# Kernel tuning notes

Measured on AMD Instinct MI355X. Metric: run time of the kernel, lower is better.

## Reference

```python
import jax, jax.numpy as jnp
import numpy as np

PENETRATION_W = 10.0
STABILITY_W = 1.0
ENERGY_W = 0.1
MIN_DIST = 0.05

B, T, N, D = 16, 100, 128, 3

def setup_inputs() -> dict:
    key = jax.random.key(0)
    k1, k2, k3 = jax.random.split(key, 3)
    trajectories = jax.random.normal(k1, (B, T, N, D), dtype=jnp.float32)
    velocities = jax.random.normal(k2, (B, T, N, D), dtype=jnp.float32)
    forces = jax.random.normal(k3, (B, T, N, D), dtype=jnp.float32)
    return {"trajectories": trajectories, "velocities": velocities, "forces": forces}

def _penetration_loss(trajectories):
    b, t, n, _ = trajectories.shape
    pos = trajectories[..., :3]                                   # [B,T,N,3]
    diff = pos[:, :, :, None, :] - pos[:, :, None, :, :]          # [B,T,N,N,3]
    d2 = jnp.sum(diff * diff, axis=-1)                            # [B,T,N,N]
    mask = jnp.triu(jnp.ones((n, n), dtype=bool), k=1)            # strictly i<j
    # avoid sqrt(0) on diagonal for safe gradients; masked out below
    dist = jnp.sqrt(jnp.where(mask, d2, 1.0))
    pen = jax.nn.relu(MIN_DIST - dist) * mask                     # [B,T,N,N]
    # original: sum over (t, i<j) of mean over batch
    total = jnp.mean(jnp.sum(pen, axis=(1, 2, 3)))
    return total / (t * n * (n - 1) / 2)

def _stability_loss(velocities):
    return jnp.mean(jnp.linalg.norm(velocities[:, -5:], axis=-1))

def _energy_loss(positions, velocities, forces):
    kinetic_start = 0.5 * jnp.mean(jnp.sum(velocities[:, 0] ** 2, axis=-1))
    kinetic_end = 0.5 * jnp.mean(jnp.sum(velocities[:, -1] ** 2, axis=-1))
    displacements = positions[:, 1:] - positions[:, :-1]
    work = jnp.mean(jnp.sum(forces[:, :-1] * displacements, axis=-1))
    return jnp.abs(kinetic_end - kinetic_start - work)

def reference(trajectories, velocities, forces):
    loss = PENETRATION_W * _penetration_loss(trajectories)
    loss = loss + STABILITY_W * _stability_loss(velocities)
    loss = loss + ENERGY_W * _energy_loss(trajectories, velocities, forces)
    return loss
```

## Files before the change

### kernel.cpp

```cpp
#include <hip/hip_runtime.h>
#include <math.h>

constexpr int B = 16, T = 100, N = 128;
constexpr float MIN_DIST  = 0.05f;
constexpr float MIN_DIST2 = MIN_DIST * MIN_DIST;

constexpr int THREADS     = 256;
constexpr int MISC_BLOCKS = 160;
constexpr int PEN_BLOCKS  = B * T / 2;
constexpr int TOTAL_BLOCKS = MISC_BLOCKS + PEN_BLOCKS;

constexpr int PER_B = T * N * 3;
constexpr int PER_T = N * 3;

constexpr int WORK_V4_PER_B = (T - 1) * N * 3 / 4;
constexpr int WORK_V4 = B * WORK_V4_PER_B;
constexpr int KE_V4_PER_SLICE = N * 3 / 4;
constexpr int KE_V4  = 2 * B * KE_V4_PER_SLICE;
constexpr int STAB_V = B * 5 * N;
constexpr int MISC_TOTAL = WORK_V4 + STAB_V + KE_V4;

constexpr int WORK_N = B * (T - 1) * N;

constexpr int WORK_OFF = 800, STAB_OFF = 960, KE0_OFF = 1120, KE1_OFF = 1280;

__device__ __forceinline__ float wave_sum(float v) {
#pragma unroll
    for (int off = 32; off > 0; off >>= 1) v += __shfl_down(v, off, 64);
    return v;
}

__global__ __launch_bounds__(THREADS) void physics_fused(
    const float* __restrict__ traj, const float* __restrict__ vel,
    const float* __restrict__ frc, float* __restrict__ ws)
{
    __shared__ float  sraw[2 * PER_T];
    __shared__ float4 spos[2 * N];
    __shared__ float  red[4][4];

    const int tid  = threadIdx.x;
    const int bid  = blockIdx.x;
    const int lane = tid & 63;
    const int wv   = tid >> 6;

    if (bid >= MISC_BLOCKS) {
        const int pb = bid - MISC_BLOCKS;
        if (tid < 192)
            ((float4*)sraw)[tid] = ((const float4*)traj)[pb * 192 + tid];
        __syncthreads();
        spos[tid] = make_float4(sraw[3 * tid], sraw[3 * tid + 1], sraw[3 * tid + 2], 0.f);
        __syncthreads();

        const int i  = tid & (N - 1);
        const int sb = (tid >> 7) * N;
        const float4 pi = spos[sb + i];
        float s = 0.f;
#pragma unroll 9
        for (int k = 1; k <= 63; ++k) {
            const int j = sb + ((i + k) & (N - 1));
            const float4 pj = spos[j];
            const float dx = pi.x - pj.x, dy = pi.y - pj.y, dz = pi.z - pj.z;
            const float d2 = dx * dx + dy * dy + dz * dz;
            const bool h = d2 < MIN_DIST2;
            if (__builtin_expect(__any(h), 0))
                if (h) s += MIN_DIST - sqrtf(d2);
        }
        {
            const float4 pj = spos[sb + ((i + 64) & (N - 1))];
            const float dx = pi.x - pj.x, dy = pi.y - pj.y, dz = pi.z - pj.z;
            const float d2 = dx * dx + dy * dy + dz * dz;
            const bool h = (d2 < MIN_DIST2) & (i < 64);
            if (__builtin_expect(__any(h), 0))
                if (h) s += MIN_DIST - sqrtf(d2);
        }
        float w = wave_sum(s);
        if (lane == 0) red[0][wv] = w;
        __syncthreads();
        if (tid == 0)
            ws[pb] = red[0][0] + red[0][1] + red[0][2] + red[0][3];
    } else {
        const int mb = bid;
        const float4* t4 = (const float4*)traj;
        const float4* f4 = (const float4*)frc;
        const float4* v4 = (const float4*)vel;
        float sw = 0.f, ss = 0.f, k0 = 0.f, k1 = 0.f;
        const int stride = MISC_BLOCKS * THREADS;
        for (int v = mb * THREADS + tid; v < MISC_TOTAL; v += stride) {
            if (v < WORK_V4) {
                const int b = v / WORK_V4_PER_B;
                const int r = v - b * WORK_V4_PER_B;
                const int base = b * (PER_B / 4) + r;
                const float4 f  = f4[base];
                const float4 t0 = t4[base];
                const float4 t1 = t4[base + PER_T / 4];
                sw += f.x * (t1.x - t0.x) + f.y * (t1.y - t0.y)
                    + f.z * (t1.z - t0.z) + f.w * (t1.w - t0.w);
            } else if (v < WORK_V4 + STAB_V) {
                const int s2 = v - WORK_V4;
                const int b  = s2 / 640;
                const int r  = s2 - b * 640;
                const int e  = b * PER_B + 95 * PER_T + r * 3;
                const float vx = vel[e], vy = vel[e + 1], vz = vel[e + 2];
                ss += sqrtf(vx * vx + vy * vy + vz * vz);
            } else {
                const int s2    = v - WORK_V4 - STAB_V;
                const int which = s2 / 1536;
                const int rr    = s2 - which * 1536;
                const int b     = rr / KE_V4_PER_SLICE;
                const int r     = rr - b * KE_V4_PER_SLICE;
                const float4 q  = v4[b * (PER_B / 4) + which * (99 * PER_T / 4) + r];
                const float k   = q.x * q.x + q.y * q.y + q.z * q.z + q.w * q.w;
                if (which) k1 += k; else k0 += k;
            }
        }
        float vals[4] = {sw, ss, k0, k1};
#pragma unroll
        for (int vv = 0; vv < 4; ++vv) {
            const float w = wave_sum(vals[vv]);
            if (lane == 0) red[vv][wv] = w;
        }
        __syncthreads();
        if (tid == 0) {
            ws[WORK_OFF + mb] = red[0][0] + red[0][1] + red[0][2] + red[0][3];
            ws[STAB_OFF + mb] = red[1][0] + red[1][1] + red[1][2] + red[1][3];
            ws[KE0_OFF  + mb] = red[2][0] + red[2][1] + red[2][2] + red[2][3];
            ws[KE1_OFF  + mb] = red[3][0] + red[3][1] + red[3][2] + red[3][3];
        }
    }
}

__global__ __launch_bounds__(256) void physics_finalize(
    const float* __restrict__ ws, float* __restrict__ out)
{
    __shared__ float redP[4], redM[4];
    const int tid = threadIdx.x, lane = tid & 63, wv = tid >> 6;

    float p = 0.f;
    for (int i = tid; i < PEN_BLOCKS; i += 256) p += ws[i];

    const int base = WORK_OFF + 160 * wv;
    float m = ws[base + lane] + ws[base + 64 + lane]
            + (lane < 32 ? ws[base + 128 + lane] : 0.f);

    p = wave_sum(p);
    m = wave_sum(m);
    if (lane == 0) { redP[wv] = p; redM[wv] = m; }
    __syncthreads();

    if (tid == 0) {
        const float pen = redP[0] + redP[1] + redP[2] + redP[3];
        const float wk = redM[0], st = redM[1], k0 = redM[2], k1 = redM[3];
        const float pen_loss  = pen / (float)((long long)B * T * (N * (N - 1) / 2));
        const float stab_loss = st / (float)STAB_V;
        const float ke_s = 0.5f * k0 / (float)(B * N);
        const float ke_e = 0.5f * k1 / (float)(B * N);
        const float work = wk / (float)WORK_N;
        out[0] = 10.0f * pen_loss + stab_loss + 0.1f * fabsf(ke_e - ke_s - work);
    }
}

extern "C" void kernel_launch(void* const* d_in, const int* in_sizes, int n_in,
                              void* d_out, int out_size, void* d_ws, size_t ws_size,
                              hipStream_t stream) {
    const float* traj = (const float*)d_in[0];
    const float* vel  = (const float*)d_in[1];
    const float* frc  = (const float*)d_in[2];
    float* out = (float*)d_out;
    float* ws  = (float*)d_ws;

    physics_fused<<<TOTAL_BLOCKS, THREADS, 0, stream>>>(traj, vel, frc, ws);
    physics_finalize<<<1, 256, 0, stream>>>(ws, out);
}
```

Baseline: 68.80 us.

## Register-tile 4x4 particle blocks per lane, one timestep per block

Each penetration block now handles a single timestep instead of two, doubling the block count. Every lane keeps four particles in registers and compares them against a partner group of four. Partner groups are assigned by a rotation scheme across waves, and the intra-group pairs are handled separately. A 4x4 minimum-distance check gates the exact penalty path, which cuts LDS loads per pair and the number of wave-vote branches. The cost is more blocks with less work each, plus more complex pair-coverage logic that must count each i<j pair exactly once.

```diff
diff --git a/kernel.cpp b/kernel.cpp
--- a/kernel.cpp
+++ b/kernel.cpp
@@ -7,7 +7,7 @@
 
 constexpr int THREADS     = 256;
 constexpr int MISC_BLOCKS = 160;
-constexpr int PEN_BLOCKS  = B * T / 2;
+constexpr int PEN_BLOCKS  = B * T;
 constexpr int TOTAL_BLOCKS = MISC_BLOCKS + PEN_BLOCKS;
 
 constexpr int PER_B = T * N * 3;
@@ -22,7 +22,7 @@
 
 constexpr int WORK_N = B * (T - 1) * N;
 
-constexpr int WORK_OFF = 800, STAB_OFF = 960, KE0_OFF = 1120, KE1_OFF = 1280;
+constexpr int WORK_OFF = 1600, STAB_OFF = 1760, KE0_OFF = 1920, KE1_OFF = 2080;
 
 __device__ __forceinline__ float wave_sum(float v) {
 #pragma unroll
@@ -34,8 +34,8 @@
     const float* __restrict__ traj, const float* __restrict__ vel,
     const float* __restrict__ frc, float* __restrict__ ws)
 {
-    __shared__ float  sraw[2 * PER_T];
-    __shared__ float4 spos[2 * N];
+    __shared__ float  sraw[PER_T];
+    __shared__ float4 spos[N];
     __shared__ float  red[4][4];
 
     const int tid  = threadIdx.x;
@@ -45,34 +45,70 @@
 
     if (bid >= MISC_BLOCKS) {
         const int pb = bid - MISC_BLOCKS;
-        if (tid < 192)
-            ((float4*)sraw)[tid] = ((const float4*)traj)[pb * 192 + tid];
-        __syncthreads();
-        spos[tid] = make_float4(sraw[3 * tid], sraw[3 * tid + 1], sraw[3 * tid + 2], 0.f);
-        __syncthreads();
-
-        const int i  = tid & (N - 1);
-        const int sb = (tid >> 7) * N;
-        const float4 pi = spos[sb + i];
+        if (tid < PER_T / 4)
+            ((float4*)sraw)[tid] = ((const float4*)traj)[pb * (PER_T / 4) + tid];
+        __syncthreads();
+        if (tid < N)
+            spos[tid] = make_float4(sraw[3 * tid], sraw[3 * tid + 1], sraw[3 * tid + 2], 0.f);
+        __syncthreads();
+
+        const int t = lane & 31;
+        const int h = lane >> 5;
+        float4 own[4];
+#pragma unroll
+        for (int p = 0; p < 4; ++p) own[p] = spos[4 * t + p];
+
         float s = 0.f;
-#pragma unroll 9
-        for (int k = 1; k <= 63; ++k) {
-            const int j = sb + ((i + k) & (N - 1));
-            const float4 pj = spos[j];
-            const float dx = pi.x - pj.x, dy = pi.y - pj.y, dz = pi.z - pj.z;
-            const float d2 = dx * dx + dy * dy + dz * dz;
-            const bool h = d2 < MIN_DIST2;
-            if (__builtin_expect(__any(h), 0))
-                if (h) s += MIN_DIST - sqrtf(d2);
-        }
-        {
-            const float4 pj = spos[sb + ((i + 64) & (N - 1))];
-            const float dx = pi.x - pj.x, dy = pi.y - pj.y, dz = pi.z - pj.z;
-            const float d2 = dx * dx + dy * dy + dz * dz;
-            const bool h = (d2 < MIN_DIST2) & (i < 64);
-            if (__builtin_expect(__any(h), 0))
-                if (h) s += MIN_DIST - sqrtf(d2);
-        }
+#pragma unroll
+        for (int it = 0; it < 2; ++it) {
+            const int m = 4 * wv + 2 * h + 1 + it;
+            const int u = (t + m) & 31;
+            const bool valid = (m < 16) | (t < 16);
+            float4 part[4];
+#pragma unroll
+            for (int p = 0; p < 4; ++p) part[p] = spos[4 * u + p];
+            float dmin = 1e30f;
+#pragma unroll
+            for (int p = 0; p < 4; ++p)
+#pragma unroll
+                for (int q = 0; q < 4; ++q) {
+                    const float dx = own[p].x - part[q].x;
+                    const float dy = own[p].y - part[q].y;
+                    const float dz = own[p].z - part[q].z;
+                    dmin = fminf(dmin, dx * dx + dy * dy + dz * dz);
+                }
+            const bool hit = valid & (dmin < MIN_DIST2);
+            if (__builtin_expect(__any(hit), 0)) {
+#pragma unroll
+                for (int p = 0; p < 4; ++p)
+#pragma unroll
+                    for (int q = 0; q < 4; ++q) {
+                        const float dx = own[p].x - part[q].x;
+                        const float dy = own[p].y - part[q].y;
+                        const float dz = own[p].z - part[q].z;
+                        const float d2 = dx * dx + dy * dy + dz * dz;
+                        if (valid && d2 < MIN_DIST2) s += MIN_DIST - sqrtf(d2);
+                    }
+            }
+        }
+        if (wv == 0) {
+            const float4 a0 = h ? own[1] : own[0], b0 = h ? own[2] : own[1];
+            const float4 a1 = h ? own[1] : own[0], b1 = h ? own[3] : own[2];
+            const float4 a2 = h ? own[2] : own[0], b2 = h ? own[3] : own[3];
+            float dx = a0.x - b0.x, dy = a0.y - b0.y, dz = a0.z - b0.z;
+            const float d20 = dx * dx + dy * dy + dz * dz;
+            dx = a1.x - b1.x; dy = a1.y - b1.y; dz = a1.z - b1.z;
+            const float d21 = dx * dx + dy * dy + dz * dz;
+            dx = a2.x - b2.x; dy = a2.y - b2.y; dz = a2.z - b2.z;
+            const float d22 = dx * dx + dy * dy + dz * dz;
+            const float dmin = fminf(d20, fminf(d21, d22));
+            if (__builtin_expect(__any(dmin < MIN_DIST2), 0)) {
+                if (d20 < MIN_DIST2) s += MIN_DIST - sqrtf(d20);
+                if (d21 < MIN_DIST2) s += MIN_DIST - sqrtf(d21);
+                if (d22 < MIN_DIST2) s += MIN_DIST - sqrtf(d22);
+            }
+        }
+
         float w = wave_sum(s);
         if (lane == 0) red[0][wv] = w;
         __syncthreads();
```

Result: no change. 69.13 us (+0.5%).
